# Kernel tuning notes

Measured on AMD Instinct MI355X. Metric: run time of the kernel, lower is better.

Reference implementation:

```python
import jax, jax.numpy as jnp
import numpy as np

DIM = 768
N_HEADS = 12
HEAD_DIM = DIM // N_HEADS

def setup_inputs() -> dict:
    key = jax.random.key(0)
    ks = jax.random.split(key, 5)
    B, N = 8, 1024
    s = 0.02
    x = jax.random.normal(ks[0], (B, N, DIM), dtype=jnp.float32)
    W_qkv = jax.random.normal(ks[1], (DIM, 3 * DIM), dtype=jnp.float32) * s
    b_qkv = jnp.zeros((3 * DIM,), dtype=jnp.float32)
    W_proj = jax.random.normal(ks[2], (DIM, DIM), dtype=jnp.float32) * s
    b_proj = jnp.zeros((DIM,), dtype=jnp.float32)
    return {"x": x, "W_qkv": W_qkv, "b_qkv": b_qkv, "W_proj": W_proj, "b_proj": b_proj}

def reference(x, W_qkv, b_qkv, W_proj, b_proj):
    B, N, D = x.shape
    qkv = x @ W_qkv + b_qkv                                   # [B,N,3D]
    qkv = qkv.reshape(B, N, 3, N_HEADS, HEAD_DIM)
    q, k, v = qkv[:, :, 0], qkv[:, :, 1], qkv[:, :, 2]        # [B,N,H,hd]
    q = q.transpose(0, 2, 1, 3)                               # [B,H,N,hd]
    k = k.transpose(0, 2, 1, 3)
    v = v.transpose(0, 2, 1, 3)
    scores = jnp.einsum('bhqd,bhkd->bhqk', q, k) / jnp.sqrt(jnp.float32(HEAD_DIM))
    attn = jax.nn.softmax(scores, axis=-1)
    out = jnp.einsum('bhqk,bhkd->bhqd', attn, v)              # [B,H,N,hd]
    out = out.transpose(0, 2, 1, 3).reshape(B, N, D)
    return out @ W_proj + b_proj
```

## Files before the change

kernel.cpp:

```cpp
#include <hip/hip_runtime.h>
#include <hip/hip_bf16.h>


typedef __bf16 bf16x8 __attribute__((ext_vector_type(8)));
typedef float f32x4 __attribute__((ext_vector_type(4)));

#define MFMA16(a, b, c) __builtin_amdgcn_mfma_f32_16x16x32_bf16(a, b, c, 0, 0, 0)

#if defined(__has_builtin) && __has_builtin(__builtin_amdgcn_exp2f)
#define EXP2(x) __builtin_amdgcn_exp2f(x)
#else
#define EXP2(x) exp2f(x)
#endif

__device__ inline __bf16 to_bf16(float f) {
  __hip_bfloat16 h = __float2bfloat16(f);
  return *reinterpret_cast<__bf16*>(&h);
}

__device__ __forceinline__ void gload16(const void* g, void* l) {
  __builtin_amdgcn_global_load_lds(
      (const __attribute__((address_space(1))) unsigned int*)(unsigned long long)g,
      (__attribute__((address_space(3))) unsigned int*)(unsigned long long)l,
      16, 0, 0);
}

__global__ void ws_diag_kernel(float* out, int n, float val) {
  int i = blockIdx.x * 256 + threadIdx.x;
  if (i < n) out[i] = val;
}

__global__ __launch_bounds__(256) void convert_x_kernel(
    const float* __restrict__ x, __hip_bfloat16* __restrict__ xc, int n8) {
  int i = blockIdx.x * 256 + threadIdx.x;
  if (i >= n8) return;
  float4 a = ((const float4*)x)[i * 2], b = ((const float4*)x)[i * 2 + 1];
  __hip_bfloat16 o[8] = {__float2bfloat16(a.x), __float2bfloat16(a.y),
                         __float2bfloat16(a.z), __float2bfloat16(a.w),
                         __float2bfloat16(b.x), __float2bfloat16(b.y),
                         __float2bfloat16(b.z), __float2bfloat16(b.w)};
  *(int4*)(xc + (size_t)i * 8) = *(const int4*)o;
}

__global__ void convert_transpose_kernel(const float* __restrict__ W,
                                         __hip_bfloat16* __restrict__ Wt,
                                         int rows, int cols) {
  __shared__ __hip_bfloat16 tile[32][33];
  const int tc = blockIdx.x * 32, tr = blockIdx.y * 32;
  const int tx = threadIdx.x, ty = threadIdx.y;
#pragma unroll
  for (int i = 0; i < 4; ++i) {
    int r = ty + i * 8;
    tile[r][tx] = __float2bfloat16(W[(size_t)(tr + r) * cols + tc + tx]);
  }
  __syncthreads();
#pragma unroll
  for (int i = 0; i < 4; ++i) {
    int r = ty + i * 8;
    Wt[(size_t)(tc + r) * rows + tr + tx] = tile[tx][r];
  }
}

__global__ __launch_bounds__(256) void vtrans_kernel(
    const __hip_bfloat16* __restrict__ Vrow, __hip_bfloat16* __restrict__ Vt) {
  constexpr int LP = 72;
  __shared__ __bf16 tile[64 * LP];
  const int tid = threadIdx.x;
  const int bh = blockIdx.x;
  const int n0 = blockIdx.y * 64;
  const size_t base = (size_t)bh << 16;
#pragma unroll
  for (int i = 0; i < 2; ++i) {
    int s = tid + 256 * i;
    int r = s >> 3, c8 = (s & 7) * 8;
    *(int4*)(&tile[r * LP + c8]) =
        *(const int4*)(Vrow + base + (size_t)(n0 + r) * 64 + c8);
  }
  __syncthreads();
#pragma unroll
  for (int i = 0; i < 2; ++i) {
    int s = tid + 256 * i;
    int d = s >> 3, n8 = (s & 7) * 8;
    __bf16 o[8];
#pragma unroll
    for (int j = 0; j < 8; ++j) o[j] = tile[(n8 + j) * LP + d];
    *(int4*)(Vt + base + ((size_t)d << 10) + n0 + n8) = *(const int4*)o;
  }
}

constexpr int GK = 768;

__global__ __launch_bounds__(256) void gemm_qkv_kernel(
    const __hip_bfloat16* __restrict__ A,
    const __hip_bfloat16* __restrict__ Bt,
    const float* __restrict__ bias,
    __hip_bfloat16* __restrict__ Qw,
    __hip_bfloat16* __restrict__ Kw,
    __hip_bfloat16* __restrict__ Vw) {
  __shared__ __align__(16) __bf16 As[128 * 32];
  __shared__ __align__(16) __bf16 Bs[128 * 32];
  const int tid = threadIdx.x;
  const int lane = tid & 63, wave = tid >> 6;
  const int wr = wave >> 1, wc = wave & 1;
  const int m0 = blockIdx.x * 128, n0 = blockIdx.y * 128;
  const int fr = lane & 15, q4 = lane >> 4;

  const int r4 = lane >> 2, c8 = (lane & 3) * 8;
  const __hip_bfloat16* ga0 = A + (size_t)(m0 + wave * 32 + r4) * GK + c8;
  const __hip_bfloat16* gb0 = Bt + (size_t)(n0 + wave * 32 + r4) * GK + c8;
  __bf16* la0 = &As[wave * 1024];
  __bf16* lb0 = &Bs[wave * 1024];

  f32x4 acc[4][4] = {};

  for (int kt = 0; kt < GK / 32; ++kt) {
    __syncthreads();
    gload16(ga0 + kt * 32, la0);
    gload16(ga0 + kt * 32 + 16 * GK, la0 + 512);
    gload16(gb0 + kt * 32, lb0);
    gload16(gb0 + kt * 32 + 16 * GK, lb0 + 512);
    __syncthreads();
    bf16x8 af[4], bfr[4];
#pragma unroll
    for (int i = 0; i < 4; ++i)
      af[i] = *(const bf16x8*)(&As[(wr * 64 + i * 16 + fr) * 32 + q4 * 8]);
#pragma unroll
    for (int j = 0; j < 4; ++j)
      bfr[j] = *(const bf16x8*)(&Bs[(wc * 64 + j * 16 + fr) * 32 + q4 * 8]);
#pragma unroll
    for (int i = 0; i < 4; ++i)
#pragma unroll
      for (int j = 0; j < 4; ++j)
        acc[i][j] = MFMA16(af[i], bfr[j], acc[i][j]);
  }

#pragma unroll
  for (int j = 0; j < 4; ++j) {
    int col = n0 + wc * 64 + j * 16 + fr;
    int which = col / 768;
    int rem = col - which * 768;
    int h = rem >> 6, d = rem & 63;
    float bv = bias[col];
    __hip_bfloat16* dst = (which == 0) ? Qw : (which == 1) ? Kw : Vw;
    float scale = (which == 0) ? 0.18033688011112042f : 1.0f;
#pragma unroll
    for (int i = 0; i < 4; ++i) {
#pragma unroll
      for (int r = 0; r < 4; ++r) {
        int row = m0 + wr * 64 + i * 16 + q4 * 4 + r;
        int bb = row >> 10, nn = row & 1023;
        float v = (acc[i][j][r] + bv) * scale;
        dst[(((size_t)(bb * 12 + h) * 1024 + nn) << 6) + d] = __float2bfloat16(v);
      }
    }
  }
}

__global__ __launch_bounds__(256) void gemm_proj_kernel(
    const __hip_bfloat16* __restrict__ A,
    const __hip_bfloat16* __restrict__ Bt,
    const float* __restrict__ bias,
    float* __restrict__ out) {
  __shared__ __align__(16) __bf16 As[128 * 32];
  __shared__ __align__(16) __bf16 Bs[128 * 32];
  const int tid = threadIdx.x;
  const int lane = tid & 63, wave = tid >> 6;
  const int wr = wave >> 1, wc = wave & 1;
  const int m0 = blockIdx.x * 128, n0 = blockIdx.y * 128;
  const int fr = lane & 15, q4 = lane >> 4;

  const int r4 = lane >> 2, c8 = (lane & 3) * 8;
  const __hip_bfloat16* ga0 = A + (size_t)(m0 + wave * 32 + r4) * GK + c8;
  const __hip_bfloat16* gb0 = Bt + (size_t)(n0 + wave * 32 + r4) * GK + c8;
  __bf16* la0 = &As[wave * 1024];
  __bf16* lb0 = &Bs[wave * 1024];

  f32x4 acc[4][4] = {};

  for (int kt = 0; kt < GK / 32; ++kt) {
    __syncthreads();
    gload16(ga0 + kt * 32, la0);
    gload16(ga0 + kt * 32 + 16 * GK, la0 + 512);
    gload16(gb0 + kt * 32, lb0);
    gload16(gb0 + kt * 32 + 16 * GK, lb0 + 512);
    __syncthreads();
    bf16x8 af[4], bfr[4];
#pragma unroll
    for (int i = 0; i < 4; ++i)
      af[i] = *(const bf16x8*)(&As[(wr * 64 + i * 16 + fr) * 32 + q4 * 8]);
#pragma unroll
    for (int j = 0; j < 4; ++j)
      bfr[j] = *(const bf16x8*)(&Bs[(wc * 64 + j * 16 + fr) * 32 + q4 * 8]);
#pragma unroll
    for (int i = 0; i < 4; ++i)
#pragma unroll
      for (int j = 0; j < 4; ++j)
        acc[i][j] = MFMA16(af[i], bfr[j], acc[i][j]);
  }

#pragma unroll
  for (int j = 0; j < 4; ++j) {
    int col = n0 + wc * 64 + j * 16 + fr;
    float bv = bias[col];
#pragma unroll
    for (int i = 0; i < 4; ++i) {
#pragma unroll
      for (int r = 0; r < 4; ++r) {
        int row = m0 + wr * 64 + i * 16 + q4 * 4 + r;
        out[(size_t)row * 768 + col] = acc[i][j][r] + bv;
      }
    }
  }
}

__global__ __launch_bounds__(512) void attn_kernel(
    const __hip_bfloat16* __restrict__ Qw,
    const __hip_bfloat16* __restrict__ Kw,
    const __hip_bfloat16* __restrict__ Vt,
    __hip_bfloat16* __restrict__ O) {
  constexpr int LP = 72;
  __shared__ __bf16 Qs[128 * LP];
  __shared__ __bf16 Ks[64 * LP];
  __shared__ __bf16 Vts[64 * LP];
  const int tid = threadIdx.x;
  const int lane = tid & 63, wave = tid >> 6;
  const int fr = lane & 15, q4 = lane >> 4;
  const int bh = blockIdx.x % 96, qt = blockIdx.x / 96;
  const __hip_bfloat16* Qb = Qw + ((size_t)bh * 1024 + qt * 128) * 64;
  const __hip_bfloat16* Kb = Kw + (size_t)bh * 65536;
  const __hip_bfloat16* Vb = Vt + (size_t)bh * 65536;

#pragma unroll
  for (int i = 0; i < 2; ++i) {
    int s = tid + 512 * i;
    int row = s >> 3, c = (s & 7) * 8;
    *(int4*)(&Qs[row * LP + c]) = *(const int4*)(Qb + row * 64 + c);
  }
  __syncthreads();
  bf16x8 qf[2];
#pragma unroll
  for (int ks = 0; ks < 2; ++ks)
    qf[ks] = *(const bf16x8*)(&Qs[(wave * 16 + fr) * LP + ks * 32 + q4 * 8]);

  float l_i = 0.f;
  f32x4 accO[4] = {};

  const int sc8 = tid & 7;
  const int sbase = ((sc8 >> 2) << 5) | ((sc8 & 1) << 4) | (((sc8 >> 1) & 1) << 2);

  for (int kt = 0; kt < 16; ++kt) {
    const int row = tid >> 3, c = (tid & 7) * 8;
    int4 kreg = *(const int4*)(Kb + (size_t)(kt * 64 + row) * 64 + c);
    int4 vreg = *(const int4*)(Vb + ((size_t)row << 10) + kt * 64 + c);
    __syncthreads();
    *(int4*)(&Ks[row * LP + c]) = kreg;
    int2 lo = make_int2(vreg.x, vreg.y);
    int2 hi = make_int2(vreg.z, vreg.w);
    *(int2*)(&Vts[row * LP + sbase]) = lo;
    *(int2*)(&Vts[row * LP + sbase + 8]) = hi;
    __syncthreads();

    f32x4 scT[4];
#pragma unroll
    for (int nt = 0; nt < 4; ++nt) {
      bf16x8 kf0 = *(const bf16x8*)(&Ks[(nt * 16 + fr) * LP + q4 * 8]);
      bf16x8 kf1 = *(const bf16x8*)(&Ks[(nt * 16 + fr) * LP + 32 + q4 * 8]);
      f32x4 z = {};
      z = MFMA16(kf0, qf[0], z);
      scT[nt] = MFMA16(kf1, qf[1], z);
    }

    float rs = 0.f;
#pragma unroll
    for (int nt = 0; nt < 4; ++nt)
#pragma unroll
      for (int r = 0; r < 4; ++r) {
        float p = EXP2(scT[nt][r]);
        scT[nt][r] = p;
        rs += p;
      }
    l_i += rs;

#pragma unroll
    for (int ks = 0; ks < 2; ++ks) {
      bf16x8 pf;
#pragma unroll
      for (int e = 0; e < 4; ++e) {
        pf[e] = to_bf16(scT[2 * ks][e]);
        pf[4 + e] = to_bf16(scT[2 * ks + 1][e]);
      }
#pragma unroll
      for (int dt = 0; dt < 4; ++dt) {
        bf16x8 vf = *(const bf16x8*)(&Vts[(dt * 16 + fr) * LP + ks * 32 + q4 * 8]);
        accO[dt] = MFMA16(pf, vf, accO[dt]);
      }
    }
  }

  l_i += __shfl_xor(l_i, 16, 64);
  l_i += __shfl_xor(l_i, 32, 64);
  float lrow[4];
#pragma unroll
  for (int r = 0; r < 4; ++r) lrow[r] = __shfl(l_i, q4 * 4 + r, 64);

  const int h = bh % 12, bb = bh / 12;
#pragma unroll
  for (int dt = 0; dt < 4; ++dt)
#pragma unroll
    for (int r = 0; r < 4; ++r) {
      int row = bb * 1024 + qt * 128 + wave * 16 + q4 * 4 + r;
      int col = h * 64 + dt * 16 + fr;
      O[(size_t)row * 768 + col] = __float2bfloat16(accO[dt][r] / lrow[r]);
    }
}

extern "C" void kernel_launch(void* const* d_in, const int* in_sizes, int n_in,
                              void* d_out, int out_size, void* d_ws, size_t ws_size,
                              hipStream_t stream) {
  const float* x     = (const float*)d_in[0];
  const float* Wqkv  = (const float*)d_in[1];
  const float* bqkv  = (const float*)d_in[2];
  const float* Wproj = (const float*)d_in[3];
  const float* bproj = (const float*)d_in[4];
  float* out = (float*)d_out;

  constexpr size_t NEEDED = 55050240;
  if (ws_size < NEEDED) {
    ws_diag_kernel<<<(out_size + 255) / 256, 256, 0, stream>>>(
        out, out_size, (float)(ws_size >> 20));
    return;
  }

  char* ws = (char*)d_ws;
  __hip_bfloat16* WqkvT  = (__hip_bfloat16*)(ws);
  __hip_bfloat16* WprojT = (__hip_bfloat16*)(ws + 3538944);
  __hip_bfloat16* Qw     = (__hip_bfloat16*)(ws + 4718592);
  __hip_bfloat16* Kw     = (__hip_bfloat16*)(ws + 17301504);
  __hip_bfloat16* Vrow   = (__hip_bfloat16*)(ws + 29884416);
  __hip_bfloat16* xc     = (__hip_bfloat16*)(ws + 42467328);
  __hip_bfloat16* Vt     = xc;
  __hip_bfloat16* attnO  = Vrow;

  convert_x_kernel<<<3072, 256, 0, stream>>>(x, xc, 786432);
  convert_transpose_kernel<<<dim3(72, 24), dim3(32, 8), 0, stream>>>(
      Wqkv, WqkvT, 768, 2304);
  convert_transpose_kernel<<<dim3(24, 24), dim3(32, 8), 0, stream>>>(
      Wproj, WprojT, 768, 768);
  gemm_qkv_kernel<<<dim3(64, 18), 256, 0, stream>>>(xc, WqkvT, bqkv, Qw, Kw, Vrow);
  vtrans_kernel<<<dim3(96, 16), 256, 0, stream>>>(Vrow, Vt);
  attn_kernel<<<dim3(96 * 8), 512, 0, stream>>>(Qw, Kw, Vt, attnO);
  gemm_proj_kernel<<<dim3(64, 6), 256, 0, stream>>>(attnO, WprojT, bproj, out);
}
```

Baseline: 195.1 us.

## Widen GEMM K-tile to 64 with XOR-swizzled LDS and prefetch attention K/V

Both GEMM kernels now stage 64-wide K tiles instead of 32, which halves the number of barrier pairs per output tile. The LDS layout uses an XOR swizzle on 16-byte chunks to avoid bank conflicts on the fragment reads. The attention kernel issues the global loads for the next K/V tile right after the barriers, so they overlap the current tile's MFMA and softmax work. The cost is twice the LDS per GEMM block and extra registers held across the loop in attention.

```diff
diff --git a/kernel.cpp b/kernel.cpp
--- a/kernel.cpp
+++ b/kernel.cpp
@@ -97,41 +97,50 @@
     __hip_bfloat16* __restrict__ Qw,
     __hip_bfloat16* __restrict__ Kw,
     __hip_bfloat16* __restrict__ Vw) {
-  __shared__ __align__(16) __bf16 As[128 * 32];
-  __shared__ __align__(16) __bf16 Bs[128 * 32];
+  __shared__ __align__(16) __bf16 As[128 * 64];
+  __shared__ __align__(16) __bf16 Bs[128 * 64];
   const int tid = threadIdx.x;
   const int lane = tid & 63, wave = tid >> 6;
   const int wr = wave >> 1, wc = wave & 1;
   const int m0 = blockIdx.x * 128, n0 = blockIdx.y * 128;
   const int fr = lane & 15, q4 = lane >> 4;
 
-  const int r4 = lane >> 2, c8 = (lane & 3) * 8;
-  const __hip_bfloat16* ga0 = A + (size_t)(m0 + wave * 32 + r4) * GK + c8;
-  const __hip_bfloat16* gb0 = Bt + (size_t)(n0 + wave * 32 + r4) * GK + c8;
-  __bf16* la0 = &As[wave * 1024];
-  __bf16* lb0 = &Bs[wave * 1024];
+  const int srow = tid >> 3;
+  const int gchunk = (tid & 7) ^ (srow & 7);
+  const __hip_bfloat16* ga = A + (size_t)(m0 + srow) * GK + gchunk * 8;
+  const __hip_bfloat16* gb = Bt + (size_t)(n0 + srow) * GK + gchunk * 8;
 
   f32x4 acc[4][4] = {};
 
-  for (int kt = 0; kt < GK / 32; ++kt) {
-    __syncthreads();
-    gload16(ga0 + kt * 32, la0);
-    gload16(ga0 + kt * 32 + 16 * GK, la0 + 512);
-    gload16(gb0 + kt * 32, lb0);
-    gload16(gb0 + kt * 32 + 16 * GK, lb0 + 512);
-    __syncthreads();
-    bf16x8 af[4], bfr[4];
-#pragma unroll
-    for (int i = 0; i < 4; ++i)
-      af[i] = *(const bf16x8*)(&As[(wr * 64 + i * 16 + fr) * 32 + q4 * 8]);
-#pragma unroll
-    for (int j = 0; j < 4; ++j)
-      bfr[j] = *(const bf16x8*)(&Bs[(wc * 64 + j * 16 + fr) * 32 + q4 * 8]);
-#pragma unroll
-    for (int i = 0; i < 4; ++i)
-#pragma unroll
-      for (int j = 0; j < 4; ++j)
-        acc[i][j] = MFMA16(af[i], bfr[j], acc[i][j]);
+  for (int kt = 0; kt < GK / 64; ++kt) {
+    __syncthreads();
+#pragma unroll
+    for (int g = 0; g < 4; ++g) {
+      gload16(ga + (size_t)g * 32 * GK + kt * 64, &As[g * 2048 + wave * 512]);
+      gload16(gb + (size_t)g * 32 * GK + kt * 64, &Bs[g * 2048 + wave * 512]);
+    }
+    __syncthreads();
+#pragma unroll
+    for (int kk = 0; kk < 2; ++kk) {
+      bf16x8 af[4], bfr[4];
+#pragma unroll
+      for (int i = 0; i < 4; ++i) {
+        int r = wr * 64 + i * 16 + fr;
+        int cs = (kk * 4 + q4) ^ (r & 7);
+        af[i] = *(const bf16x8*)(&As[r * 64 + cs * 8]);
+      }
+#pragma unroll
+      for (int j = 0; j < 4; ++j) {
+        int r = wc * 64 + j * 16 + fr;
+        int cs = (kk * 4 + q4) ^ (r & 7);
+        bfr[j] = *(const bf16x8*)(&Bs[r * 64 + cs * 8]);
+      }
+#pragma unroll
+      for (int i = 0; i < 4; ++i)
+#pragma unroll
+        for (int j = 0; j < 4; ++j)
+          acc[i][j] = MFMA16(af[i], bfr[j], acc[i][j]);
+    }
   }
 
 #pragma unroll
@@ -161,41 +170,50 @@
     const __hip_bfloat16* __restrict__ Bt,
     const float* __restrict__ bias,
     float* __restrict__ out) {
-  __shared__ __align__(16) __bf16 As[128 * 32];
-  __shared__ __align__(16) __bf16 Bs[128 * 32];
+  __shared__ __align__(16) __bf16 As[128 * 64];
+  __shared__ __align__(16) __bf16 Bs[128 * 64];
   const int tid = threadIdx.x;
   const int lane = tid & 63, wave = tid >> 6;
   const int wr = wave >> 1, wc = wave & 1;
   const int m0 = blockIdx.x * 128, n0 = blockIdx.y * 128;
   const int fr = lane & 15, q4 = lane >> 4;
 
-  const int r4 = lane >> 2, c8 = (lane & 3) * 8;
-  const __hip_bfloat16* ga0 = A + (size_t)(m0 + wave * 32 + r4) * GK + c8;
-  const __hip_bfloat16* gb0 = Bt + (size_t)(n0 + wave * 32 + r4) * GK + c8;
-  __bf16* la0 = &As[wave * 1024];
-  __bf16* lb0 = &Bs[wave * 1024];
+  const int srow = tid >> 3;
+  const int gchunk = (tid & 7) ^ (srow & 7);
+  const __hip_bfloat16* ga = A + (size_t)(m0 + srow) * GK + gchunk * 8;
+  const __hip_bfloat16* gb = Bt + (size_t)(n0 + srow) * GK + gchunk * 8;
 
   f32x4 acc[4][4] = {};
 
-  for (int kt = 0; kt < GK / 32; ++kt) {
-    __syncthreads();
-    gload16(ga0 + kt * 32, la0);
-    gload16(ga0 + kt * 32 + 16 * GK, la0 + 512);
-    gload16(gb0 + kt * 32, lb0);
-    gload16(gb0 + kt * 32 + 16 * GK, lb0 + 512);
-    __syncthreads();
-    bf16x8 af[4], bfr[4];
-#pragma unroll
-    for (int i = 0; i < 4; ++i)
-      af[i] = *(const bf16x8*)(&As[(wr * 64 + i * 16 + fr) * 32 + q4 * 8]);
-#pragma unroll
-    for (int j = 0; j < 4; ++j)
-      bfr[j] = *(const bf16x8*)(&Bs[(wc * 64 + j * 16 + fr) * 32 + q4 * 8]);
-#pragma unroll
-    for (int i = 0; i < 4; ++i)
-#pragma unroll
-      for (int j = 0; j < 4; ++j)
-        acc[i][j] = MFMA16(af[i], bfr[j], acc[i][j]);
+  for (int kt = 0; kt < GK / 64; ++kt) {
+    __syncthreads();
+#pragma unroll
+    for (int g = 0; g < 4; ++g) {
+      gload16(ga + (size_t)g * 32 * GK + kt * 64, &As[g * 2048 + wave * 512]);
+      gload16(gb + (size_t)g * 32 * GK + kt * 64, &Bs[g * 2048 + wave * 512]);
+    }
+    __syncthreads();
+#pragma unroll
+    for (int kk = 0; kk < 2; ++kk) {
+      bf16x8 af[4], bfr[4];
+#pragma unroll
+      for (int i = 0; i < 4; ++i) {
+        int r = wr * 64 + i * 16 + fr;
+        int cs = (kk * 4 + q4) ^ (r & 7);
+        af[i] = *(const bf16x8*)(&As[r * 64 + cs * 8]);
+      }
+#pragma unroll
+      for (int j = 0; j < 4; ++j) {
+        int r = wc * 64 + j * 16 + fr;
+        int cs = (kk * 4 + q4) ^ (r & 7);
+        bfr[j] = *(const bf16x8*)(&Bs[r * 64 + cs * 8]);
+      }
+#pragma unroll
+      for (int i = 0; i < 4; ++i)
+#pragma unroll
+        for (int j = 0; j < 4; ++j)
+          acc[i][j] = MFMA16(af[i], bfr[j], acc[i][j]);
+    }
   }
 
 #pragma unroll
@@ -230,6 +248,10 @@
   const __hip_bfloat16* Kb = Kw + (size_t)bh * 65536;
   const __hip_bfloat16* Vb = Vt + (size_t)bh * 65536;
 
+  const int krow = tid >> 3, kc = (tid & 7) * 8;
+  int4 kreg = *(const int4*)(Kb + (size_t)krow * 64 + kc);
+  int4 vreg = *(const int4*)(Vb + ((size_t)krow << 10) + kc);
+
 #pragma unroll
   for (int i = 0; i < 2; ++i) {
     int s = tid + 512 * i;
@@ -249,16 +271,16 @@
   const int sbase = ((sc8 >> 2) << 5) | ((sc8 & 1) << 4) | (((sc8 >> 1) & 1) << 2);
 
   for (int kt = 0; kt < 16; ++kt) {
-    const int row = tid >> 3, c = (tid & 7) * 8;
-    int4 kreg = *(const int4*)(Kb + (size_t)(kt * 64 + row) * 64 + c);
-    int4 vreg = *(const int4*)(Vb + ((size_t)row << 10) + kt * 64 + c);
-    __syncthreads();
-    *(int4*)(&Ks[row * LP + c]) = kreg;
-    int2 lo = make_int2(vreg.x, vreg.y);
-    int2 hi = make_int2(vreg.z, vreg.w);
-    *(int2*)(&Vts[row * LP + sbase]) = lo;
-    *(int2*)(&Vts[row * LP + sbase + 8]) = hi;
-    __syncthreads();
+    __syncthreads();
+    *(int4*)(&Ks[krow * LP + kc]) = kreg;
+    *(int2*)(&Vts[krow * LP + sbase]) = make_int2(vreg.x, vreg.y);
+    *(int2*)(&Vts[krow * LP + sbase + 8]) = make_int2(vreg.z, vreg.w);
+    __syncthreads();
+
+    if (kt < 15) {
+      kreg = *(const int4*)(Kb + (size_t)((kt + 1) * 64 + krow) * 64 + kc);
+      vreg = *(const int4*)(Vb + ((size_t)krow << 10) + (kt + 1) * 64 + kc);
+    }
 
     f32x4 scT[4];
 #pragma unroll
```

Result: slower. 200.7 us (+2.9%).
